# Optimization experiments

Hardware: AMD Instinct MI355X
Metric: run time of the kernel (lower is better)

## Reference

```python
import jax, jax.numpy as jnp
import numpy as np

N = 50000          # nodes
E = 800000         # edges (avg degree 16)
NFEAT = 128        # dim_touched / gcn_nfeat
NHID = 96
NCLASS = 64
EXTRA = 32         # extra MLP-only features
NHID1, NHID2 = 128, 64
NN = 70            # top-k threshold rank
EPS = 1e-5         # BatchNorm1d eps


def setup_inputs() -> dict:
    key = jax.random.key(0)
    ks = jax.random.split(key, 24)
    x = jax.random.normal(ks[0], (N, NFEAT + EXTRA + 1), jnp.float32)
    grp = jax.random.randint(ks[1], (N,), 0, 2).astype(jnp.float32)
    x = x.at[:, -1].set(grp)  # last column is the group flag (target_group == 0)
    row = jax.random.randint(ks[2], (E,), 0, N, dtype=jnp.int32)
    col = jax.random.randint(ks[3], (E,), 0, N, dtype=jnp.int32)
    val = jax.random.uniform(ks[4], (E,), jnp.float32)

    def p(k, shape):
        return (jax.random.normal(k, shape, jnp.float32) * 0.05)

    return dict(
        x=x, row=row, col=col, val=val,
        W1=p(ks[5], (NFEAT, NHID)), b1=p(ks[6], (NHID,)),
        W2=p(ks[7], (NHID, NHID)), b2=p(ks[8], (NHID,)),
        W3=p(ks[9], (NHID, NHID)), b3=p(ks[10], (NHID,)),
        W4=p(ks[11], (NHID, NHID)), b4=p(ks[12], (NHID,)),
        W5=p(ks[13], (NHID, NCLASS)), b5=p(ks[14], (NCLASS,)),
        M1w=p(ks[15], (NCLASS + EXTRA, NHID1)), M1b=p(ks[16], (NHID1,)),
        M2w=p(ks[17], (NHID1, NHID2)), M2b=p(ks[18], (NHID2,)),
        M3w=p(ks[19], (NHID2, 1)), M3b=p(ks[20], (1,)),
    )


def _bn(h):
    # fresh BatchNorm1d in training mode, affine at default init (gamma=1, beta=0)
    m = jnp.mean(h, axis=0)
    v = jnp.mean((h - m) ** 2, axis=0)  # biased variance, as used for normalization
    return (h - m) * jax.lax.rsqrt(v + EPS)


def _gc(h, row, col, val, W, b):
    # GraphConvolution: spmm(adj, h @ W) + b, adj in COO form
    s = h @ W                                            # [N, out]
    msg = val[:, None] * s[col]                          # [E, out]
    agg = jax.ops.segment_sum(msg, row, num_segments=N)  # [N, out]
    return agg + b


def reference(x, row, col, val, W1, b1, W2, b2, W3, b3, W4, b4, W5, b5,
              M1w, M1b, M2w, M2b, M3w, M3b):
    h = x[:, :NFEAT]
    h = _bn(jax.nn.relu(_gc(h, row, col, val, W1, b1)))
    h = _bn(jax.nn.relu(_gc(h, row, col, val, W2, b2)))
    h = _bn(jax.nn.relu(_gc(h, row, col, val, W3, b3)))
    h = _bn(jax.nn.relu(_gc(h, row, col, val, W4, b4)))
    h = jax.nn.relu(_gc(h, row, col, val, W5, b5))        # [N, NCLASS]

    feat = jnp.concatenate([h, x[:, NFEAT:-1]], axis=1)   # [N, NCLASS+EXTRA]
    m = jax.nn.relu(feat @ M1w + M1b)
    m = jax.nn.relu(m @ M2w + M2b)
    m = m @ M3w + M3b                                     # [N, 1]

    # mask out target_group rows with the global min
    m = jnp.where(x[:, -1:] == 0.0, jnp.min(m), m)        # [N, 1]

    # top-70 threshold: value at descending rank NN
    thresh = jax.lax.top_k(m[:, 0], NN + 1)[0][NN]
    recip = jax.lax.stop_gradient(1.0 / m)                # torch reciprocal on detach()
    mask = jnp.where(m > thresh, recip, jnp.zeros_like(m))
    return m * mask
```

## Files before the change

kernel.cpp:

```cpp
#include <hip/hip_runtime.h>
#include <cstdint>
#include <cstddef>

#define XLD 161
#define GA  2048

typedef float f4u __attribute__((ext_vector_type(4), aligned(4)));
typedef float f4a __attribute__((ext_vector_type(4)));
typedef float f3u __attribute__((ext_vector_type(3), aligned(4)));
typedef float f2a __attribute__((ext_vector_type(2)));

__global__ void hist_kernel(const int* __restrict__ row, int* __restrict__ cnt, int E) {
    for (int e = blockIdx.x * blockDim.x + threadIdx.x; e < E; e += gridDim.x * blockDim.x)
        atomicAdd(&cnt[row[e]], 1);
}

__global__ __launch_bounds__(256)
void scan1_kernel(const int* __restrict__ cnt, int* __restrict__ offs,
                  int* __restrict__ bsums, int n) {
    int t = threadIdx.x;
    int gid = blockIdx.x * 256 + t;
    int v = (gid < n) ? cnt[gid] : 0;
    int x = v;
#pragma unroll
    for (int o = 1; o < 64; o <<= 1) { int y = __shfl_up(x, o); if ((t & 63) >= o) x += y; }
    __shared__ int ws[4];
    if ((t & 63) == 63) ws[t >> 6] = x;
    __syncthreads();
    int add = 0;
    for (int w = 0; w < (t >> 6); w++) add += ws[w];
    int incl = x + add;
    if (gid < n) offs[gid] = incl - v;
    if (t == 255) bsums[blockIdx.x] = incl;
}

__global__ __launch_bounds__(256)
void scan2_kernel(int* __restrict__ bsums, int nb) {
    int t = threadIdx.x;
    int v = (t < nb) ? bsums[t] : 0;
    int x = v;
#pragma unroll
    for (int o = 1; o < 64; o <<= 1) { int y = __shfl_up(x, o); if ((t & 63) >= o) x += y; }
    __shared__ int ws[4];
    if ((t & 63) == 63) ws[t >> 6] = x;
    __syncthreads();
    int add = 0;
    for (int w = 0; w < (t >> 6); w++) add += ws[w];
    if (t < nb) bsums[t] = x + add - v;
}

__global__ void scan3_kernel(int* __restrict__ offs, int* __restrict__ cursor,
                             const int* __restrict__ bsums, int n, int E) {
    int gid = blockIdx.x * 256 + threadIdx.x;
    if (gid < n) {
        int o = offs[gid] + bsums[blockIdx.x];
        offs[gid] = o;
        cursor[gid] = o;
    }
    if (gid == 0) offs[n] = E;
}

__global__ void scatter_kernel(const int* __restrict__ row, const int* __restrict__ col,
                               const float* __restrict__ val, int* __restrict__ cursor,
                               int2* __restrict__ cvA, int E) {
    for (int e = blockIdx.x * blockDim.x + threadIdx.x; e < E; e += gridDim.x * blockDim.x) {
        int r = row[e];
        int p = atomicAdd(&cursor[r], 1);
        cvA[p] = make_int2(col[e], __float_as_int(val[e]));
    }
}

template <int LC, bool WVS>
__global__ __launch_bounds__(256)
void aggP(const float* __restrict__ S, int ldS, const int* __restrict__ offs,
          const int2* __restrict__ cvA,
          float* __restrict__ Aout, float* __restrict__ vout, int n) {
    int lane = threadIdx.x & 63;
    int lg   = lane & 31;
    int grp  = threadIdx.x >> 5;
    int sh   = lane & 32;

    for (int node = blockIdx.x * 8 + grp; node < n; node += gridDim.x * 8) {
        int e0 = offs[node], e1 = offs[node + 1];
        float acc[LC];
#pragma unroll
        for (int a = 0; a < LC; a++) acc[a] = 0.f;
        float vsum = 0.f;

        for (int e = e0; e < e1; e += 32) {
            int   idx = e + lg;
            int2  cv = (idx < e1) ? cvA[idx] : make_int2(0, 0);
            int   ce = cv.x;
            float ve = __int_as_float(cv.y);
            int   cnt = min(32, e1 - e);
#pragma unroll 8
            for (int j = 0; j < cnt; j++) {
                int   c = __shfl(ce, sh + j);
                float v = __shfl(ve, sh + j);
                const float* srow = S + (size_t)c * ldS + LC * lg;
                if (LC == 3) {
                    f3u g = *(const f3u*)srow;
                    acc[0] = fmaf(v, g[0], acc[0]);
                    acc[1] = fmaf(v, g[1], acc[1]);
                    acc[2] = fmaf(v, g[2], acc[2]);
                } else {
                    f4u g = *(const f4u*)srow;
                    acc[0] = fmaf(v, g[0], acc[0]);
                    acc[1] = fmaf(v, g[1], acc[1]);
                    acc[2] = fmaf(v, g[2], acc[2]);
                    acc[3] = fmaf(v, g[3], acc[3]);
                }
                vsum += v;
            }
        }

        float* orow = Aout + (size_t)node * (32 * LC) + LC * lg;
        if (LC == 3) {
            f3u o; o[0] = acc[0]; o[1] = acc[1]; o[2] = acc[2];
            *(f3u*)orow = o;
        } else {
            f4u o; o[0] = acc[0]; o[1] = acc[1]; o[2] = acc[2]; o[3] = acc[3];
            *(f4u*)orow = o;
        }
        if (WVS && lg == 0) vout[node] = vsum;
    }
}

__global__ __launch_bounds__(256)
void aggB(const float* __restrict__ S, const int* __restrict__ offs,
          const int2* __restrict__ cvA, const float* __restrict__ bias,
          float* __restrict__ Hout, float* __restrict__ vout,
          float* __restrict__ pbuf, int n) {
    __shared__ float sS[96], sQ[96];
    int t = threadIdx.x;
    if (t < 96) { sS[t] = 0.f; sQ[t] = 0.f; }
    __syncthreads();
    int lane = t & 63, lg = lane & 31, grp = t >> 5, sh = lane & 32;
    float bb[3];
    bb[0] = bias[3 * lg]; bb[1] = bias[3 * lg + 1]; bb[2] = bias[3 * lg + 2];
    float ps[3] = {0.f, 0.f, 0.f}, pq[3] = {0.f, 0.f, 0.f};

    for (int node = blockIdx.x * 8 + grp; node < n; node += gridDim.x * 8) {
        int e0 = offs[node], e1 = offs[node + 1];
        float acc[3] = {0.f, 0.f, 0.f};
        float vsum = 0.f;
        for (int e = e0; e < e1; e += 32) {
            int   idx = e + lg;
            int2  cv = (idx < e1) ? cvA[idx] : make_int2(0, 0);
            int   ce = cv.x;
            float ve = __int_as_float(cv.y);
            int   cnt = min(32, e1 - e);
#pragma unroll 8
            for (int j = 0; j < cnt; j++) {
                int   c = __shfl(ce, sh + j);
                float v = __shfl(ve, sh + j);
                const float* srow = S + (size_t)c * 96 + 3 * lg;
                f3u g = *(const f3u*)srow;
                acc[0] = fmaf(v, g[0], acc[0]);
                acc[1] = fmaf(v, g[1], acc[1]);
                acc[2] = fmaf(v, g[2], acc[2]);
                vsum += v;
            }
        }
        float* orow = Hout + (size_t)node * 96 + 3 * lg;
        f3u o;
#pragma unroll
        for (int a = 0; a < 3; a++) {
            float v = fmaxf(acc[a] + bb[a], 0.f);
            o[a] = v;
            ps[a] += v; pq[a] += v * v;
        }
        *(f3u*)orow = o;
        if (lg == 0) vout[node] = vsum;
    }
#pragma unroll
    for (int a = 0; a < 3; a++) {
        atomicAdd(&sS[3 * lg + a], ps[a]);
        atomicAdd(&sQ[3 * lg + a], pq[a]);
    }
    __syncthreads();
    if (t < 96) {
        pbuf[(size_t)blockIdx.x * 192 + t]      = sS[t];
        pbuf[(size_t)blockIdx.x * 192 + 96 + t] = sQ[t];
    }
}

__global__ __launch_bounds__(256)
void bn_reduce(const float* __restrict__ pbuf, float* __restrict__ stats) {
    int t = threadIdx.x;
    float s = 0.f;
    if (t < 192) {
        for (int pb = blockIdx.x; pb < GA; pb += gridDim.x)
            s += pbuf[(size_t)pb * 192 + t];
        atomicAdd(&stats[t], s);
    }
}

__global__ __launch_bounds__(256)
void aggC(const float* __restrict__ S, const int* __restrict__ offs,
          const int2* __restrict__ cvA, const float* __restrict__ bias,
          const float* __restrict__ cb, const float* __restrict__ vsum,
          float* __restrict__ Hout, int n) {
    int lane = threadIdx.x & 63, lg = lane & 31, grp = threadIdx.x >> 5, sh = lane & 32;
    float bb0 = bias[2 * lg], bb1 = bias[2 * lg + 1];
    float cc0 = cb[2 * lg],   cc1 = cb[2 * lg + 1];

    for (int node = blockIdx.x * 8 + grp; node < n; node += gridDim.x * 8) {
        int e0 = offs[node], e1 = offs[node + 1];
        float a0 = 0.f, a1 = 0.f;
        for (int e = e0; e < e1; e += 32) {
            int   idx = e + lg;
            int2  cv = (idx < e1) ? cvA[idx] : make_int2(0, 0);
            int   ce = cv.x;
            float ve = __int_as_float(cv.y);
            int   cnt = min(32, e1 - e);
#pragma unroll 8
            for (int j = 0; j < cnt; j++) {
                int   c = __shfl(ce, sh + j);
                float v = __shfl(ve, sh + j);
                f2a g = *(const f2a*)(S + (size_t)c * 64 + 2 * lg);
                a0 = fmaf(v, g[0], a0);
                a1 = fmaf(v, g[1], a1);
            }
        }
        float vs = vsum[node];
        f2a o;
        o[0] = fmaxf(a0 + vs * cc0 + bb0, 0.f);
        o[1] = fmaxf(a1 + vs * cc1 + bb1, 0.f);
        *(f2a*)(Hout + (size_t)node * 64 + 2 * lg) = o;
    }
}

template <int CT>
__device__ inline void ldw(const float* p, float* wv) {
    if constexpr (CT == 4) { *(f4a*)wv = *(const f4a*)p; }
    else if constexpr (CT == 6) { *(f3u*)wv = *(const f3u*)p; *(f3u*)(wv + 3) = *(const f3u*)(p + 3); }
    else { *(f4a*)wv = *(const f4a*)p; *(f4a*)(wv + 4) = *(const f4a*)(p + 4); }
}

template <int K, int C, bool DOBN, bool HASCB, bool LIN = false, bool DOT = false>
__global__ __launch_bounds__(256)
void gemmF(const float* __restrict__ A1, int ld1, int split,
           const float* __restrict__ A2, int ld2,
           const float* __restrict__ W, const float* __restrict__ bias,
           const float* __restrict__ cbv, const float* __restrict__ vsum,
           float* __restrict__ Out, float* __restrict__ bsum,
           float* __restrict__ bsumsq, int n) {
    constexpr int CT = C / 16;
    __shared__ float Wc[16 * C];
    __shared__ float At[16][68];
    __shared__ float redS[DOBN ? C : 1];
    __shared__ float redQ[DOBN ? C : 1];

    int t  = threadIdx.x;
    int tc = t & 15, tr = t >> 4;
    int row0 = blockIdx.x * 64;

    if (DOBN && t < C) { redS[t] = 0.f; redQ[t] = 0.f; }

    int srow = t >> 2;
    int gr = row0 + srow; if (gr >= n) gr = n - 1;
    int kh = (t & 3) * 4;

    float acc[4][CT];
#pragma unroll
    for (int i = 0; i < 4; i++)
#pragma unroll
        for (int c = 0; c < CT; c++) acc[i][c] = 0.f;

    for (int kb = 0; kb < K; kb += 16) {
        __syncthreads();
        for (int i = t * 4; i < 16 * C; i += 1024)
            *(f4a*)&Wc[i] = *(const f4u*)&W[(size_t)kb * C + i];
        {
            int kg = kb + kh;
            const float* src = (kg < split) ? (A1 + (size_t)gr * ld1 + kg)
                                            : (A2 + (size_t)gr * ld2 + (kg - split));
            f4u v = *(const f4u*)src;
#pragma unroll
            for (int e = 0; e < 4; e++) At[kh + e][srow] = v[e];
        }
        __syncthreads();
#pragma unroll
        for (int kk = 0; kk < 16; kk++) {
            f4a av = *(const f4a*)&At[kk][tr * 4];
            float wv[CT];
            ldw<CT>(&Wc[kk * C + tc * CT], wv);
#pragma unroll
            for (int i = 0; i < 4; i++)
#pragma unroll
                for (int c = 0; c < CT; c++) acc[i][c] = fmaf(av[i], wv[c], acc[i][c]);
        }
    }

    if constexpr (DOT) {
        float bb2[CT], ww[CT];
#pragma unroll
        for (int c = 0; c < CT; c++) { bb2[c] = bias[tc * CT + c]; ww[c] = cbv[tc * CT + c]; }
        float b3 = vsum[0];
        float lmin = 3.4e38f;
#pragma unroll
        for (int i = 0; i < 4; i++) {
            float d = 0.f;
#pragma unroll
            for (int c = 0; c < CT; c++) d = fmaf(fmaxf(acc[i][c] + bb2[c], 0.f), ww[c], d);
            d += __shfl_xor(d, 1); d += __shfl_xor(d, 2);
            d += __shfl_xor(d, 4); d += __shfl_xor(d, 8);
            int r = row0 + tr * 4 + i;
            if (tc == 0 && r < n) {
                float mv = d + b3;
                Out[r] = mv;
                lmin = fminf(lmin, mv);
            }
        }
        __shared__ float smin[16];
        if (tc == 0) smin[tr] = lmin;
        __syncthreads();
        if (t == 0) {
            float mn = smin[0];
#pragma unroll
            for (int i2 = 1; i2 < 16; i2++) mn = fminf(mn, smin[i2]);
            unsigned u = __float_as_uint(mn);
            unsigned key = (u >> 31) ? ~u : (u | 0x80000000u);
            atomicMin((unsigned*)bsum, key);
        }
        return;
    }

    float bb[CT], cc[CT];
#pragma unroll
    for (int c = 0; c < CT; c++) {
        bb[c] = LIN ? 0.f : bias[tc * CT + c];
        cc[c] = HASCB ? cbv[tc * CT + c] : 0.f;
    }
    float ps[CT], pq[CT];
#pragma unroll
    for (int c = 0; c < CT; c++) { ps[c] = 0.f; pq[c] = 0.f; }

#pragma unroll
    for (int i = 0; i < 4; i++) {
        int r = row0 + tr * 4 + i;
        if (r < n) {
            float vs = HASCB ? vsum[r] : 0.f;
            float* o = Out + (size_t)r * C + tc * CT;
#pragma unroll
            for (int c = 0; c < CT; c++) {
                float v = acc[i][c] + vs * cc[c] + bb[c];
                if (!LIN) v = fmaxf(v, 0.f);
                o[c] = v;
                if (DOBN) { ps[c] += v; pq[c] += v * v; }
            }
        }
    }
    if (DOBN) {
#pragma unroll
        for (int c = 0; c < CT; c++) {
            ps[c] += __shfl_xor(ps[c], 16);
            ps[c] += __shfl_xor(ps[c], 32);
            pq[c] += __shfl_xor(pq[c], 16);
            pq[c] += __shfl_xor(pq[c], 32);
        }
        if ((t & 48) == 0) {
#pragma unroll
            for (int c = 0; c < CT; c++) {
                atomicAdd(&redS[tc * CT + c], ps[c]);
                atomicAdd(&redQ[tc * CT + c], pq[c]);
            }
        }
        __syncthreads();
        if (t < C) {
            atomicAdd(&bsum[t], redS[t]);
            atomicAdd(&bsumsq[t], redQ[t]);
        }
    }
}

template <int C>
__global__ __launch_bounds__(256)
void fold_kernel(const float* __restrict__ W, float* __restrict__ bsum,
                 float* __restrict__ bsumsq, float* __restrict__ Wf,
                 float* __restrict__ cb, int N) {
    __shared__ float mean[96], inv[96];
    int t = threadIdx.x;
    float rn = 1.0f / (float)N;
    if (t < 96) {
        float mu  = bsum[t] * rn;
        float var = bsumsq[t] * rn - mu * mu;
        mean[t] = mu;
        inv[t]  = rsqrtf(var + 1e-5f);
        bsum[t] = 0.f;
        bsumsq[t] = 0.f;
    }
    __syncthreads();
    for (int i = t; i < 96 * C; i += 256) {
        int k = i / C;
        Wf[i] = inv[k] * W[i];
    }
    if (t < C) {
        float s = 0.f;
        for (int k = 0; k < 96; k++) s += mean[k] * inv[k] * W[k * C + t];
        cb[t] = -s;
    }
}

__device__ inline unsigned fkey(float f) {
    unsigned u = __float_as_uint(f);
    return (u >> 31) ? ~u : (u | 0x80000000u);
}

__global__ __launch_bounds__(256)
void where_hist(const float* __restrict__ x, float* __restrict__ m,
                const unsigned* __restrict__ gmin, unsigned* __restrict__ h0, int n) {
    __shared__ unsigned lh[256];
    int t = threadIdx.x;
    lh[t] = 0u;
    __syncthreads();
    unsigned k = *gmin;
    unsigned u = (k >> 31) ? (k ^ 0x80000000u) : ~k;
    float g = __uint_as_float(u);
    for (int i = blockIdx.x * 256 + t; i < n; i += gridDim.x * 256) {
        float mv = m[i];
        if (x[(size_t)i * XLD + 160] == 0.0f) { mv = g; m[i] = mv; }
        atomicAdd(&lh[fkey(mv) >> 24], 1u);
    }
    __syncthreads();
    if (lh[t]) atomicAdd(&h0[t], lh[t]);
}

__global__ __launch_bounds__(256)
void sel_pick8(const unsigned* __restrict__ h, const unsigned* __restrict__ kres,
               int kconst, unsigned* __restrict__ outb, unsigned* __restrict__ outk) {
    int t = threadIdx.x;
    int bin = 255 - t;
    unsigned k = kres ? *kres : (unsigned)kconst;
    unsigned c = h[bin];
    unsigned x = c;
#pragma unroll
    for (int o = 1; o < 64; o <<= 1) { unsigned y = __shfl_up(x, o); if ((t & 63) >= o) x += y; }
    __shared__ unsigned ws[4];
    if ((t & 63) == 63) ws[t >> 6] = x;
    __syncthreads();
    unsigned add = 0;
    for (int w = 0; w < (t >> 6); w++) add += ws[w];
    unsigned incl = x + add, excl = incl - c;
    if (excl < k && k <= incl) { *outb = (unsigned)bin; *outk = k - excl; }
}

__global__ __launch_bounds__(256)
void sel_hist8b(const float* __restrict__ m, const unsigned* __restrict__ pick,
                unsigned* __restrict__ h1, int n) {
    __shared__ unsigned lh[256];
    int t = threadIdx.x;
    lh[t] = 0u;
    __syncthreads();
    unsigned b0 = pick[0];
    for (int i = blockIdx.x * 256 + t; i < n; i += gridDim.x * 256) {
        unsigned key = fkey(m[i]);
        if ((key >> 24) == b0) atomicAdd(&lh[(key >> 16) & 255u], 1u);
    }
    __syncthreads();
    if (lh[t]) atomicAdd(&h1[t], lh[t]);
}

__global__ void sel_collect(const float* __restrict__ m, const unsigned* __restrict__ pick,
                            unsigned* __restrict__ sbuf, unsigned* __restrict__ scnt, int n) {
    unsigned pfx = (pick[0] << 8) | pick[2];
    for (int i = blockIdx.x * blockDim.x + threadIdx.x; i < n; i += gridDim.x * blockDim.x) {
        unsigned key = fkey(m[i]);
        if ((key >> 16) == pfx) sbuf[atomicAdd(scnt, 1u)] = key;
    }
}

__global__ __launch_bounds__(1024)
void sel_final(const unsigned* __restrict__ sbuf, const unsigned* __restrict__ scnt,
               const unsigned* __restrict__ pick, float* __restrict__ thresh) {
    __shared__ unsigned hist[256];
    __shared__ unsigned spfx;
    __shared__ int skk;
    int t = threadIdx.x;
    int ns = (int)*scnt;
    if (t == 0) { spfx = ((pick[0] << 8) | pick[2]) << 16; skk = (int)pick[3]; }
    __syncthreads();
    for (int pass = 0; pass < 2; ++pass) {
        if (t < 256) hist[t] = 0u;
        __syncthreads();
        int shift = 8 - 8 * pass;
        unsigned pfxmask = (pass == 0) ? 0xFFFF0000u : 0xFFFFFF00u;
        unsigned pfx = spfx;
        for (int i = t; i < ns; i += 1024) {
            unsigned key = sbuf[i];
            if ((key & pfxmask) == pfx) atomicAdd(&hist[(key >> shift) & 255u], 1u);
        }
        __syncthreads();
        if (t == 0) {
            int cum = 0, kk = skk, chosen = 0;
            for (int b = 255; b >= 0; b--) {
                cum += (int)hist[b];
                if (cum >= kk) { chosen = b; kk -= (cum - (int)hist[b]); break; }
            }
            spfx = pfx | ((unsigned)chosen << shift);
            skk = kk;
        }
        __syncthreads();
    }
    if (t == 0) {
        unsigned key = spfx;
        unsigned u = (key >> 31) ? (key ^ 0x80000000u) : ~key;
        *thresh = __uint_as_float(u);
    }
}

__global__ void mask_kernel(const float* __restrict__ m, const float* __restrict__ thresh,
                            float* __restrict__ out, int n) {
    int i = blockIdx.x * blockDim.x + threadIdx.x;
    if (i < n) {
        float t = *thresh, v = m[i];
        out[i] = (v > t) ? v * (1.0f / v) : 0.0f;
    }
}

extern "C" void kernel_launch(void* const* d_in, const int* in_sizes, int n_in,
                              void* d_out, int out_size, void* d_ws, size_t ws_size,
                              hipStream_t stream) {
    const float* x   = (const float*)d_in[0];
    const int*   row = (const int*)d_in[1];
    const int*   col = (const int*)d_in[2];
    const float* val = (const float*)d_in[3];
    const float* W1  = (const float*)d_in[4];
    const float* b1  = (const float*)d_in[5];
    const float* W2  = (const float*)d_in[6];
    const float* b2  = (const float*)d_in[7];
    const float* W3  = (const float*)d_in[8];
    const float* b3  = (const float*)d_in[9];
    const float* W4  = (const float*)d_in[10];
    const float* b4  = (const float*)d_in[11];
    const float* W5  = (const float*)d_in[12];
    const float* b5  = (const float*)d_in[13];
    const float* M1w = (const float*)d_in[14];
    const float* M1b = (const float*)d_in[15];
    const float* M2w = (const float*)d_in[16];
    const float* M2b = (const float*)d_in[17];
    const float* M3w = (const float*)d_in[18];
    const float* M3b = (const float*)d_in[19];

    const int n = in_sizes[0] / XLD;
    const int E = in_sizes[1];

    char* ws = (char*)d_ws;
    size_t off = 0;
    auto carve = [&](size_t bytes) -> void* {
        void* p = ws + off;
        off = (off + bytes + 255) & ~(size_t)255;
        return p;
    };
    int*      offs   = (int*)carve((size_t)(n + 1) * 4);
    int*      cursor = (int*)carve((size_t)n * 4);
    int*      bsums  = (int*)carve(256 * 4);
    int2*     cvA    = (int2*)carve((size_t)E * 8);
    float*    h      = (float*)carve((size_t)n * 96 * 4);
    float*    big    = (float*)carve((size_t)n * 128 * 4);
    float*    Wf     = (float*)carve(96 * 96 * 4);
    float*    stats  = (float*)carve(192 * 4);
    float*    cb     = (float*)carve(96 * 4);
    float*    vsum   = (float*)carve((size_t)n * 4);
    float*    m      = (float*)carve((size_t)n * 4);
    unsigned* gmin   = (unsigned*)carve(4);
    float*    thresh = (float*)carve(4);
    unsigned* h0     = (unsigned*)carve(256 * 4);
    unsigned* h1     = (unsigned*)carve(256 * 4);
    unsigned* sbuf   = (unsigned*)carve((size_t)n * 4);
    unsigned* scnt   = (unsigned*)carve(4);
    unsigned* pick   = (unsigned*)carve(16);
    float*    pbuf   = (float*)carve((size_t)GA * 192 * 4);
    float* bsum   = stats;
    float* bsumsq = stats + 96;

    hipMemsetAsync(cursor, 0, (size_t)n * 4, stream);
    hipMemsetAsync(stats, 0, 192 * 4, stream);
    hipMemsetAsync(gmin, 0xFF, 4, stream);
    hipMemsetAsync(h0, 0, 256 * 4, stream);
    hipMemsetAsync(h1, 0, 256 * 4, stream);
    hipMemsetAsync(scnt, 0, 4, stream);

    const int nb = (n + 255) / 256;
    hist_kernel<<<2048, 256, 0, stream>>>(row, cursor, E);
    scan1_kernel<<<nb, 256, 0, stream>>>(cursor, offs, bsums, n);
    scan2_kernel<<<1, 256, 0, stream>>>(bsums, nb);
    scan3_kernel<<<nb, 256, 0, stream>>>(offs, cursor, bsums, n, E);
    scatter_kernel<<<2048, 256, 0, stream>>>(row, col, val, cursor, cvA, E);

    const int gB = (n + 63) / 64;

    gemmF<128, 96, false, false, true><<<gB, 256, 0, stream>>>(x, XLD, 128, x, XLD,
        W1, b1, nullptr, nullptr, big, bsum, bsumsq, n);
    aggB<<<GA, 256, 0, stream>>>(big, offs, cvA, b1, h, vsum, pbuf, n);
    bn_reduce<<<64, 256, 0, stream>>>(pbuf, stats);

    fold_kernel<96><<<1, 256, 0, stream>>>(W2, bsum, bsumsq, Wf, cb, n);
    aggP<3, false><<<GA, 256, 0, stream>>>(h, 96, offs, cvA, big, nullptr, n);
    gemmF<96, 96, true, true><<<gB, 256, 0, stream>>>(big, 96, 96, big, 96,
        Wf, b2, cb, vsum, h, bsum, bsumsq, n);

    fold_kernel<96><<<1, 256, 0, stream>>>(W3, bsum, bsumsq, Wf, cb, n);
    aggP<3, false><<<GA, 256, 0, stream>>>(h, 96, offs, cvA, big, nullptr, n);
    gemmF<96, 96, true, true><<<gB, 256, 0, stream>>>(big, 96, 96, big, 96,
        Wf, b3, cb, vsum, h, bsum, bsumsq, n);

    fold_kernel<96><<<1, 256, 0, stream>>>(W4, bsum, bsumsq, Wf, cb, n);
    aggP<3, false><<<GA, 256, 0, stream>>>(h, 96, offs, cvA, big, nullptr, n);
    gemmF<96, 96, true, true><<<gB, 256, 0, stream>>>(big, 96, 96, big, 96,
        Wf, b4, cb, vsum, h, bsum, bsumsq, n);

    fold_kernel<64><<<1, 256, 0, stream>>>(W5, bsum, bsumsq, Wf, cb, n);
    gemmF<96, 64, false, false, true><<<gB, 256, 0, stream>>>(h, 96, 96, h, 96,
        Wf, b5, nullptr, nullptr, big, bsum, bsumsq, n);
    aggC<<<GA, 256, 0, stream>>>(big, offs, cvA, b5, cb, vsum, h, n);

    gemmF<96, 128, false, false><<<gB, 256, 0, stream>>>(h, 64, 64, x + 128, XLD,
        M1w, M1b, nullptr, nullptr, big, bsum, bsumsq, n);
    gemmF<128, 64, false, false, false, true><<<gB, 256, 0, stream>>>(big, 128, 128, big, 128,
        M2w, M2b, M3w, M3b, m, (float*)gmin, nullptr, n);

    where_hist<<<64, 256, 0, stream>>>(x, m, gmin, h0, n);

    sel_pick8<<<1, 256, 0, stream>>>(h0, nullptr, 71, &pick[0], &pick[1]);
    sel_hist8b<<<64, 256, 0, stream>>>(m, pick, h1, n);
    sel_pick8<<<1, 256, 0, stream>>>(h1, &pick[1], 0, &pick[2], &pick[3]);
    sel_collect<<<64, 256, 0, stream>>>(m, pick, sbuf, scnt, n);
    sel_final<<<1, 1024, 0, stream>>>(sbuf, scnt, pick, thresh);

    mask_kernel<<<(n + 255) / 256, 256, 0, stream>>>(m, thresh, (float*)d_out, n);
}
```

Baseline: 724.7 us.

## Fuse middle-layer aggregation with folded-BN GEMM and ReLU epilogue

For layers 2-4, a new aggG kernel gathers neighbour features per node, multiplies the aggregate by the BN-folded weight held transposed in shared memory, and adds bias, ReLU and the BatchNorm partial sums in the same kernel. This replaces the separate aggP and gemmF launches and the round trip of the intermediate aggregate through global memory. The fold kernel gains a transposed, padded output layout, and ping-pong activation buffers replace h/big. The scatter step now writes the packed (col, val) pair with a nontemporal store. The per-node GEMM runs on scalar FMAs with a 40KB shared weight tile per block, which may limit occupancy and compute throughput compared with the tiled GEMM.

Result: slower. 797.3 us (+10.0%).

```diff
diff --git a/kernel.cpp b/kernel.cpp
--- a/kernel.cpp
+++ b/kernel.cpp
@@ -4,6 +4,7 @@
 
 #define XLD 161
 #define GA  2048
+#define GG  1536
 
 typedef float f4u __attribute__((ext_vector_type(4), aligned(4)));
 typedef float f4a __attribute__((ext_vector_type(4)));
@@ -66,7 +67,9 @@
     for (int e = blockIdx.x * blockDim.x + threadIdx.x; e < E; e += gridDim.x * blockDim.x) {
         int r = row[e];
         int p = atomicAdd(&cursor[r], 1);
-        cvA[p] = make_int2(col[e], __float_as_int(val[e]));
+        long long packed = ((long long)(unsigned)__float_as_int(val[e]) << 32)
+                         | (unsigned)col[e];
+        __builtin_nontemporal_store(packed, (long long*)(cvA + p));
     }
 }
 
@@ -186,11 +189,93 @@
 }
 
 __global__ __launch_bounds__(256)
-void bn_reduce(const float* __restrict__ pbuf, float* __restrict__ stats) {
-    int t = threadIdx.x;
-    float s = 0.f;
+void aggG(const float* __restrict__ Sin, const int* __restrict__ offs,
+          const int2* __restrict__ cvA, const float* __restrict__ WfT,
+          const float* __restrict__ cb, const float* __restrict__ bias,
+          const float* __restrict__ vsum, float* __restrict__ Hout,
+          float* __restrict__ pbuf, int n) {
+    __shared__ float WT[96 * 104];
+    __shared__ float stg[8][96];
+    __shared__ float sS[96], sQ[96];
+
+    int t = threadIdx.x;
+    for (int i = t * 4; i < 96 * 104; i += 1024)
+        *(f4a*)&WT[i] = *(const f4u*)&WfT[i];
+    if (t < 96) { sS[t] = 0.f; sQ[t] = 0.f; }
+    __syncthreads();
+
+    int lane = t & 63, lg = lane & 31, slot = t >> 5, sh = lane & 32;
+    float bb[3], cc[3];
+#pragma unroll
+    for (int a = 0; a < 3; a++) { bb[a] = bias[3 * lg + a]; cc[a] = cb[3 * lg + a]; }
+    float ps[3] = {0.f, 0.f, 0.f}, pq[3] = {0.f, 0.f, 0.f};
+
+    for (int node = blockIdx.x * 8 + slot; node < n; node += gridDim.x * 8) {
+        int e0 = offs[node], e1 = offs[node + 1];
+        float acc[3] = {0.f, 0.f, 0.f};
+        for (int e = e0; e < e1; e += 32) {
+            int   idx = e + lg;
+            int2  cv = (idx < e1) ? cvA[idx] : make_int2(0, 0);
+            int   ce = cv.x;
+            float ve = __int_as_float(cv.y);
+            int   cnt = min(32, e1 - e);
+#pragma unroll 8
+            for (int j = 0; j < cnt; j++) {
+                int   c = __shfl(ce, sh + j);
+                float v = __shfl(ve, sh + j);
+                f3u g = *(const f3u*)(Sin + (size_t)c * 96 + 3 * lg);
+                acc[0] = fmaf(v, g[0], acc[0]);
+                acc[1] = fmaf(v, g[1], acc[1]);
+                acc[2] = fmaf(v, g[2], acc[2]);
+            }
+        }
+        stg[slot][3 * lg]     = acc[0];
+        stg[slot][3 * lg + 1] = acc[1];
+        stg[slot][3 * lg + 2] = acc[2];
+        __builtin_amdgcn_wave_barrier();
+        float o0 = 0.f, o1 = 0.f, o2 = 0.f;
+        const float* wr = &WT[(3 * lg) * 104];
+#pragma unroll
+        for (int kc = 0; kc < 96; kc += 4) {
+            f4a sv = *(const f4a*)&stg[slot][kc];
+            f4a w0 = *(const f4a*)&wr[kc];
+            f4a w1 = *(const f4a*)&wr[104 + kc];
+            f4a w2 = *(const f4a*)&wr[208 + kc];
+#pragma unroll
+            for (int q = 0; q < 4; q++) {
+                o0 = fmaf(sv[q], w0[q], o0);
+                o1 = fmaf(sv[q], w1[q], o1);
+                o2 = fmaf(sv[q], w2[q], o2);
+            }
+        }
+        __builtin_amdgcn_wave_barrier();
+        float vs = vsum[node];
+        f3u o;
+        o[0] = fmaxf(o0 + vs * cc[0] + bb[0], 0.f);
+        o[1] = fmaxf(o1 + vs * cc[1] + bb[1], 0.f);
+        o[2] = fmaxf(o2 + vs * cc[2] + bb[2], 0.f);
+        *(f3u*)(Hout + (size_t)node * 96 + 3 * lg) = o;
+#pragma unroll
+        for (int a = 0; a < 3; a++) { ps[a] += o[a]; pq[a] += o[a] * o[a]; }
+    }
+#pragma unroll
+    for (int a = 0; a < 3; a++) {
+        atomicAdd(&sS[3 * lg + a], ps[a]);
+        atomicAdd(&sQ[3 * lg + a], pq[a]);
+    }
+    __syncthreads();
+    if (t < 96) {
+        pbuf[(size_t)blockIdx.x * 192 + t]      = sS[t];
+        pbuf[(size_t)blockIdx.x * 192 + 96 + t] = sQ[t];
+    }
+}
+
+__global__ __launch_bounds__(256)
+void bn_reduce(const float* __restrict__ pbuf, float* __restrict__ stats, int nb) {
+    int t = threadIdx.x;
     if (t < 192) {
-        for (int pb = blockIdx.x; pb < GA; pb += gridDim.x)
+        float s = 0.f;
+        for (int pb = blockIdx.x; pb < nb; pb += gridDim.x)
             s += pbuf[(size_t)pb * 192 + t];
         atomicAdd(&stats[t], s);
     }
@@ -375,7 +460,7 @@
     }
 }
 
-template <int C>
+template <int C, bool TR>
 __global__ __launch_bounds__(256)
 void fold_kernel(const float* __restrict__ W, float* __restrict__ bsum,
                  float* __restrict__ bsumsq, float* __restrict__ Wf,
@@ -393,8 +478,9 @@
     }
     __syncthreads();
     for (int i = t; i < 96 * C; i += 256) {
-        int k = i / C;
-        Wf[i] = inv[k] * W[i];
+        int k = i / C, j = i - k * C;
+        if (TR) Wf[(size_t)j * 104 + k] = inv[k] * W[i];
+        else    Wf[i] = inv[k] * W[i];
     }
     if (t < C) {
         float s = 0.f;
@@ -557,9 +643,9 @@
     int*      cursor = (int*)carve((size_t)n * 4);
     int*      bsums  = (int*)carve(256 * 4);
     int2*     cvA    = (int2*)carve((size_t)E * 8);
-    float*    h      = (float*)carve((size_t)n * 96 * 4);
-    float*    big    = (float*)carve((size_t)n * 128 * 4);
-    float*    Wf     = (float*)carve(96 * 96 * 4);
+    float*    hA     = (float*)carve((size_t)n * 128 * 4);
+    float*    hB     = (float*)carve((size_t)n * 128 * 4);
+    float*    Wf     = (float*)carve(96 * 104 * 4);
     float*    stats  = (float*)carve(192 * 4);
     float*    cb     = (float*)carve(96 * 4);
     float*    vsum   = (float*)carve((size_t)n * 4);
@@ -592,33 +678,30 @@
     const int gB = (n + 63) / 64;
 
     gemmF<128, 96, false, false, true><<<gB, 256, 0, stream>>>(x, XLD, 128, x, XLD,
-        W1, b1, nullptr, nullptr, big, bsum, bsumsq, n);
-    aggB<<<GA, 256, 0, stream>>>(big, offs, cvA, b1, h, vsum, pbuf, n);
-    bn_reduce<<<64, 256, 0, stream>>>(pbuf, stats);
-
-    fold_kernel<96><<<1, 256, 0, stream>>>(W2, bsum, bsumsq, Wf, cb, n);
-    aggP<3, false><<<GA, 256, 0, stream>>>(h, 96, offs, cvA, big, nullptr, n);
-    gemmF<96, 96, true, true><<<gB, 256, 0, stream>>>(big, 96, 96, big, 96,
-        Wf, b2, cb, vsum, h, bsum, bsumsq, n);
-
-    fold_kernel<96><<<1, 256, 0, stream>>>(W3, bsum, bsumsq, Wf, cb, n);
-    aggP<3, false><<<GA, 256, 0, stream>>>(h, 96, offs, cvA, big, nullptr, n);
-    gemmF<96, 96, true, true><<<gB, 256, 0, stream>>>(big, 96, 96, big, 96,
-        Wf, b3, cb, vsum, h, bsum, bsumsq, n);
-
-    fold_kernel<96><<<1, 256, 0, stream>>>(W4, bsum, bsumsq, Wf, cb, n);
-    aggP<3, false><<<GA, 256, 0, stream>>>(h, 96, offs, cvA, big, nullptr, n);
-    gemmF<96, 96, true, true><<<gB, 256, 0, stream>>>(big, 96, 96, big, 96,
-        Wf, b4, cb, vsum, h, bsum, bsumsq, n);
-
-    fold_kernel<64><<<1, 256, 0, stream>>>(W5, bsum, bsumsq, Wf, cb, n);
-    gemmF<96, 64, false, false, true><<<gB, 256, 0, stream>>>(h, 96, 96, h, 96,
-        Wf, b5, nullptr, nullptr, big, bsum, bsumsq, n);
-    aggC<<<GA, 256, 0, stream>>>(big, offs, cvA, b5, cb, vsum, h, n);
-
-    gemmF<96, 128, false, false><<<gB, 256, 0, stream>>>(h, 64, 64, x + 128, XLD,
-        M1w, M1b, nullptr, nullptr, big, bsum, bsumsq, n);
-    gemmF<128, 64, false, false, false, true><<<gB, 256, 0, stream>>>(big, 128, 128, big, 128,
+        W1, b1, nullptr, nullptr, hB, bsum, bsumsq, n);
+    aggB<<<GA, 256, 0, stream>>>(hB, offs, cvA, b1, hA, vsum, pbuf, n);
+    bn_reduce<<<64, 256, 0, stream>>>(pbuf, stats, GA);
+
+    fold_kernel<96, true><<<1, 256, 0, stream>>>(W2, bsum, bsumsq, Wf, cb, n);
+    aggG<<<GG, 256, 0, stream>>>(hA, offs, cvA, Wf, cb, b2, vsum, hB, pbuf, n);
+    bn_reduce<<<64, 256, 0, stream>>>(pbuf, stats, GG);
+
+    fold_kernel<96, true><<<1, 256, 0, stream>>>(W3, bsum, bsumsq, Wf, cb, n);
+    aggG<<<GG, 256, 0, stream>>>(hB, offs, cvA, Wf, cb, b3, vsum, hA, pbuf, n);
+    bn_reduce<<<64, 256, 0, stream>>>(pbuf, stats, GG);
+
+    fold_kernel<96, true><<<1, 256, 0, stream>>>(W4, bsum, bsumsq, Wf, cb, n);
+    aggG<<<GG, 256, 0, stream>>>(hA, offs, cvA, Wf, cb, b4, vsum, hB, pbuf, n);
+    bn_reduce<<<64, 256, 0, stream>>>(pbuf, stats, GG);
+
+    fold_kernel<64, false><<<1, 256, 0, stream>>>(W5, bsum, bsumsq, Wf, cb, n);
+    gemmF<96, 64, false, false, true><<<gB, 256, 0, stream>>>(hB, 96, 96, hB, 96,
+        Wf, b5, nullptr, nullptr, hA, bsum, bsumsq, n);
+    aggC<<<GA, 256, 0, stream>>>(hA, offs, cvA, b5, cb, vsum, hB, n);
+
+    gemmF<96, 128, false, false><<<gB, 256, 0, stream>>>(hB, 64, 64, x + 128, XLD,
+        M1w, M1b, nullptr, nullptr, hA, bsum, bsumsq, n);
+    gemmF<128, 64, false, false, false, true><<<gB, 256, 0, stream>>>(hA, 128, 128, hA, 128,
         M2w, M2b, M3w, M3b, m, (float*)gmin, nullptr, n);
 
     where_hist<<<64, 256, 0, stream>>>(x, m, gmin, h0, n);
```
